# Kernel tuning notes

Measured on AMD Instinct MI355X. Metric: run time of the kernel, lower is better.

## Reference

```python
import jax, jax.numpy as jnp
import numpy as np

N_HEADS = 16

def _rotate_half(t):
    d = t.shape[-1] // 2
    return jnp.concatenate([-t[..., d:], t[..., :d]], axis=-1)

def _apply_rope(t, cos, sin):
    # t: [B,S,H,dh], cos/sin: [S,1,dh] broadcast over B and H
    return t * cos + _rotate_half(t) * sin

def setup_inputs() -> dict:
    key = jax.random.key(0)
    ks = jax.random.split(key, 7)
    B, S, D = 2, 2048, 2048
    dh = D // N_HEADS
    scale = 1.0 / np.sqrt(D)
    return {
        "x": jax.random.normal(ks[0], (B, S, D), dtype=jnp.float32),
        "rope_cos": jax.random.uniform(ks[1], (S, dh), dtype=jnp.float32),
        "rope_sin": jax.random.uniform(ks[2], (S, dh), dtype=jnp.float32),
        "Wq": jax.random.normal(ks[3], (D, D), dtype=jnp.float32) * scale,
        "Wk": jax.random.normal(ks[4], (D, D), dtype=jnp.float32) * scale,
        "Wv": jax.random.normal(ks[5], (D, D), dtype=jnp.float32) * scale,
        "Wo": jax.random.normal(ks[6], (D, D), dtype=jnp.float32) * scale,
    }

def reference(x, rope_cos, rope_sin, Wq, Wk, Wv, Wo):
    B, S, D = x.shape
    H = N_HEADS
    dh = D // H
    # QKV projections (nn.Linear: x @ W.T), reshape to heads
    q = (x @ Wq.T).reshape(B, S, H, dh)
    k = (x @ Wk.T).reshape(B, S, H, dh)
    v = (x @ Wv.T).reshape(B, S, H, dh)
    cos = rope_cos[:, None, :]  # [S,1,dh]
    sin = rope_sin[:, None, :]
    q = _apply_rope(q, cos, sin)
    k = _apply_rope(k, cos, sin)
    # Attention: [B,H,S,S] scores, scaled softmax
    scores = jnp.einsum("bqhd,bkhd->bhqk", q, k) / jnp.sqrt(jnp.asarray(dh, dtype=x.dtype))
    probs = jax.nn.softmax(scores, axis=-1)
    out = jnp.einsum("bhqk,bkhd->bqhd", probs, v).reshape(B, S, D)
    return out @ Wo.T
```

## Files before the change

kernel.cpp:

```cpp
#include <hip/hip_runtime.h>
#include <hip/hip_bf16.h>

typedef unsigned short u16;
typedef __bf16 bf16x8 __attribute__((ext_vector_type(8)));
typedef float f32x4 __attribute__((ext_vector_type(4)));

__device__ __forceinline__ float bf2f(u16 u) {
  union { unsigned int i; float f; } v; v.i = ((unsigned int)u) << 16; return v.f;
}
__device__ __forceinline__ u16 f2bf(float f) {
  union { float f; unsigned int i; } v; v.f = f;
  unsigned int r = v.i + 0x7fffu + ((v.i >> 16) & 1u);
  return (u16)(r >> 16);
}
__device__ __forceinline__ unsigned cvtpk(float lo, float hi) {
  unsigned r;
  asm("v_cvt_pk_bf16_f32 %0, %1, %2" : "=v"(r) : "v"(lo), "v"(hi));
  return r;
}

__device__ __forceinline__ void async_load16(void* lds, const void* g) {
  __builtin_amdgcn_global_load_lds((const __attribute__((address_space(1))) void*)g,
                                   (__attribute__((address_space(3))) void*)lds, 16, 0, 0);
}

__global__ void convert_all(const float* __restrict__ x, const float* __restrict__ Wq,
                            const float* __restrict__ Wk, const float* __restrict__ Wv,
                            const float* __restrict__ Wo, u16* __restrict__ xb,
                            u16* __restrict__ Wqkb, u16* __restrict__ Wvb,
                            u16* __restrict__ Wob) {
  int bid = blockIdx.x;
  const float* src;
  u16* dst;
  int off;
  if (bid < 8192)       { src = x;  dst = xb;              off = bid; }
  else if (bid < 12288) { src = Wq; dst = Wqkb;            off = bid - 8192; }
  else if (bid < 16384) { src = Wk; dst = Wqkb + 4194304;  off = bid - 12288; }
  else if (bid < 20480) { src = Wv; dst = Wvb;             off = bid - 16384; }
  else                  { src = Wo; dst = Wob;             off = bid - 20480; }
  int i = off * 1024 + threadIdx.x * 4;
  float4 v = *(const float4*)(src + i);
  ushort4 o;
  o.x = f2bf(v.x); o.y = f2bf(v.y); o.z = f2bf(v.z); o.w = f2bf(v.w);
  *(ushort4*)(dst + i) = o;
}

template <int BMHALF, int ROPE, int OUT_F32>
__device__ __forceinline__ void gemm_pipe_body(const u16* __restrict__ A,
                                               const u16* __restrict__ Bm,
                                               void* __restrict__ C, int M, int N, int K,
                                               int tm, int tn, u16* lds,
                                               const float* __restrict__ cosb,
                                               const float* __restrict__ sinb,
                                               float qscale) {
  constexpr int MIc = BMHALF / 16;
  constexpr int SUBU16 = (BMHALF == 128) ? 16384 : 12288;
  constexpr int BOFF = (BMHALF == 128) ? 8192 : 4096;
  const int t = threadIdx.x;
  const int w = t >> 6, l = t & 63;
  const int wm = w >> 2, wn = w & 3;
  const int lr = l & 15, lh = l >> 4;
  const size_t row0 = (size_t)tm * (2 * BMHALF), col0 = (size_t)tn * 256;
  const u16* Ag = A + row0 * K;
  const u16* Bg = Bm + col0 * K;

  const int ra = t >> 2;
  const int kcs = ((t & 3) << 3) ^ ((ra & 6) << 2);
  auto stage = [&](int s) {
    u16* dst = lds + (s & 3) * SUBU16;
    const size_t koff = (size_t)s * 32 + kcs;
    if constexpr (BMHALF == 128) {
      async_load16(dst + t * 8,         Ag + (size_t)ra * K + koff);
      async_load16(dst + 4096 + t * 8,  Ag + (size_t)(ra + 128) * K + koff);
      async_load16(dst + 8192 + t * 8,  Bg + (size_t)ra * K + koff);
      async_load16(dst + 12288 + t * 8, Bg + (size_t)(ra + 128) * K + koff);
    } else {
      async_load16(dst + t * 8,         Ag + (size_t)ra * K + koff);
      async_load16(dst + 4096 + t * 8,  Bg + (size_t)ra * K + koff);
      async_load16(dst + 8192 + t * 8,  Bg + (size_t)(ra + 128) * K + koff);
    }
  };
  const int swl = (lh * 8) ^ ((lr & 6) << 2);
  auto read_af = [&](bf16x8* dst, int s) {
    const u16* sub = lds + (s & 3) * SUBU16;
#pragma unroll
    for (int mi = 0; mi < MIc; ++mi)
      dst[mi] = *reinterpret_cast<const bf16x8*>(sub + (wm * BMHALF + mi * 16 + lr) * 32 + swl);
  };
  auto read_bfv = [&](bf16x8* dst, int s) {
    const u16* sub = lds + (s & 3) * SUBU16 + BOFF;
#pragma unroll
    for (int ni = 0; ni < 4; ++ni) {
      int colf = ROPE ? ((wn >> 1) * 128 + (wn & 1) * 32 + (ni >> 1) * 64 + (ni & 1) * 16)
                      : (wn * 64 + ni * 16);
      dst[ni] = *reinterpret_cast<const bf16x8*>(sub + (colf + lr) * 32 + swl);
    }
  };

  f32x4 acc[MIc][4];
#pragma unroll
  for (int i = 0; i < MIc; ++i)
#pragma unroll
    for (int j = 0; j < 4; ++j) acc[i][j] = (f32x4){0.f, 0.f, 0.f, 0.f};

  const int NK = K >> 5;
  bf16x8 afA[MIc], afB[MIc], bfvA[4], bfvB[4];

  stage(0); stage(1); stage(2);
  if constexpr (BMHALF == 128) asm volatile("s_waitcnt vmcnt(8)" ::: "memory");
  else                         asm volatile("s_waitcnt vmcnt(6)" ::: "memory");
  __builtin_amdgcn_s_barrier();
  asm volatile("" ::: "memory");
  read_af(afA, 0);
  read_bfv(bfvA, 0);

  auto pipestep = [&](int s, bf16x8* curA, bf16x8* curB, bf16x8* nxtA, bf16x8* nxtB) {
    if (s + 2 < NK) {
      if constexpr (BMHALF == 128) asm volatile("s_waitcnt vmcnt(4)" ::: "memory");
      else                         asm volatile("s_waitcnt vmcnt(3)" ::: "memory");
    } else {
      asm volatile("s_waitcnt vmcnt(0)" ::: "memory");
    }
    __builtin_amdgcn_s_barrier();
    asm volatile("" ::: "memory");
    if (s + 3 < NK) stage(s + 3);
    if (s + 1 < NK) {
      read_af(nxtA, s + 1);
      read_bfv(nxtB, s + 1);
    }
    __builtin_amdgcn_s_setprio(1);
#pragma unroll
    for (int mi = 0; mi < MIc; ++mi)
#pragma unroll
      for (int ni = 0; ni < 4; ++ni)
        acc[mi][ni] = __builtin_amdgcn_mfma_f32_16x16x32_bf16(curA[mi], curB[ni], acc[mi][ni], 0, 0, 0);
    __builtin_amdgcn_s_setprio(0);
  };

  for (int s = 0; s < NK; s += 2) {
    pipestep(s,     afA, bfvA, afB, bfvB);
    pipestep(s + 1, afB, bfvB, afA, bfvA);
  }

  if constexpr (ROPE) {
    float scale = (2 * tn + (wn >> 1)) < 16 ? qscale : 1.0f;
    size_t colbase = col0 + (wn >> 1) * 128;
#pragma unroll
    for (int mi = 0; mi < MIc; ++mi)
#pragma unroll
      for (int r = 0; r < 4; ++r) {
        size_t row = row0 + wm * BMHALF + mi * 16 + lh * 4 + r;
        int si = (int)(row & 2047);
        const float* cr = cosb + si * 128;
        const float* sr = sinb + si * 128;
#pragma unroll
        for (int ni = 0; ni < 2; ++ni) {
          int dlo = (wn & 1) * 32 + ni * 16 + lr;
          float v0 = acc[mi][ni][r];
          float v1 = acc[mi][ni + 2][r];
          float o0 = (v0 * cr[dlo] - v1 * sr[dlo]) * scale;
          float o1 = (v1 * cr[64 + dlo] + v0 * sr[64 + dlo]) * scale;
          ((u16*)C)[row * N + colbase + dlo]      = f2bf(o0);
          ((u16*)C)[row * N + colbase + 64 + dlo] = f2bf(o1);
        }
      }
  } else {
#pragma unroll
    for (int mi = 0; mi < MIc; ++mi)
#pragma unroll
      for (int ni = 0; ni < 4; ++ni)
#pragma unroll
        for (int r = 0; r < 4; ++r) {
          size_t row = row0 + wm * BMHALF + mi * 16 + lh * 4 + r;
          size_t col = col0 + wn * 64 + ni * 16 + lr;
          float v = acc[mi][ni][r];
          if (OUT_F32)
            ((float*)C)[row * N + col] = v;
          else
            ((u16*)C)[row * N + col] = f2bf(v);
        }
  }
}

__global__ __launch_bounds__(512, 2)
void gemm_qkv256(const u16* __restrict__ xb, const u16* __restrict__ Wqkb,
                 const u16* __restrict__ Wvb, u16* __restrict__ QKb, u16* __restrict__ VTb,
                 const float* __restrict__ cosb, const float* __restrict__ sinb,
                 float qscale) {
  __shared__ __align__(16) u16 lds[4 * 16384];
  int bid = blockIdx.x;
  if (bid < 256) {
    int swz = (bid & 7) * 32 + (bid >> 3);
    gemm_pipe_body<128, 1, 0>(xb, Wqkb, QKb, 4096, 4096, 2048, swz >> 4, swz & 15, lds,
                              cosb, sinb, qscale);
  } else {
    int b2 = bid - 256;
    int swz = (b2 & 7) * 32 + (b2 >> 3);
    gemm_pipe_body<64, 0, 0>(Wvb, xb, VTb, 2048, 4096, 2048, swz >> 4, swz & 15, lds,
                             nullptr, nullptr, 0.f);
  }
}

__global__ __launch_bounds__(512, 2)
void gemm_o(const u16* __restrict__ Ob, const u16* __restrict__ Wob, float* __restrict__ out) {
  __shared__ __align__(16) u16 lds[4 * 16384];
  int bid = blockIdx.x;
  int swz = (bid & 7) * 32 + (bid >> 3);
  gemm_pipe_body<64, 0, 1>(Ob, Wob, (void*)out, 4096, 2048, 2048, swz >> 3, swz & 7, lds,
                           nullptr, nullptr, 0.f);
}

__global__ __launch_bounds__(256, 2)
void attn_kernel(const u16* __restrict__ QKb, const u16* __restrict__ VT,
                 u16* __restrict__ Ob) {
  __shared__ __align__(16) u16 sK[2][64 * 128];
  __shared__ __align__(16) u16 sV[2][128 * 64];
  __shared__ __align__(16) u16 sP[4][32 * 64];

  int id = blockIdx.x;
  int swz = (id & 7) * 64 + (id >> 3);
  int bh = swz >> 4;
  int qb = swz & 15;
  int b = bh >> 4, h = bh & 15;
  int t = threadIdx.x, w = t >> 6, l = t & 63;
  int lr = l & 15, lh = l >> 4;
  int lr7 = lr & 7;
  int q0 = qb * 128;

  const u16* Kbase = QKb + (size_t)(b * 2048) * 4096 + 2048 + h * 128;
  const u16* Vbase = VT + (size_t)(h * 128) * 4096 + b * 2048;
  u16* sPw = sP[w];

  bf16x8 aq[2][4];
#pragma unroll
  for (int qf = 0; qf < 2; ++qf) {
    size_t qrow = (size_t)(b * 2048 + q0 + w * 32 + qf * 16 + lr) * 4096 + h * 128;
#pragma unroll
    for (int c = 0; c < 4; ++c)
      aq[qf][c] = *reinterpret_cast<const bf16x8*>(QKb + qrow + c * 32 + lh * 8);
  }

  f32x4 zero = {0.f, 0.f, 0.f, 0.f};
  f32x4 acc_o[2][8];
#pragma unroll
  for (int qf = 0; qf < 2; ++qf)
#pragma unroll
    for (int d = 0; d < 8; ++d) acc_o[qf][d] = zero;
  float m_row[2] = {-1e30f, -1e30f};
  float l_row[2] = {0.f, 0.f};

  auto stage = [&](int buf, int kt2) {
    const u16* Kt = Kbase + (size_t)(kt2 * 64) * 4096;
    const u16* Vt = Vbase + kt2 * 64;
#pragma unroll
    for (int it = 0; it < 4; ++it) {
      int o = it * 4096 + t * 16;
      int rowK = o >> 8;
      int cbK = (o & 255) ^ ((rowK & 7) << 4);
      async_load16((u16*)sK[buf] + (o >> 1), Kt + (size_t)rowK * 4096 + (cbK >> 1));
      int rowV = o >> 7;
      int cbV = (o & 127) ^ ((rowV & 7) << 4);
      async_load16((u16*)sV[buf] + (o >> 1), Vt + (size_t)rowV * 4096 + (cbV >> 1));
    }
  };

  stage(0, 0);
  __syncthreads();
  int cur = 0;

  for (int kt = 0; kt < 32; ++kt) {
    if (kt < 31) stage(cur ^ 1, kt + 1);

    const u16* sKc = sK[cur];
    const u16* sVc = sV[cur];

    f32x4 sacc[2][4];
#pragma unroll
    for (int qf = 0; qf < 2; ++qf)
#pragma unroll
      for (int g = 0; g < 4; ++g) sacc[qf][g] = zero;
#pragma unroll
    for (int g = 0; g < 4; ++g) {
      int row = g * 16 + lr;
      int xr = lr7 << 4;
#pragma unroll
      for (int c = 0; c < 4; ++c) {
        int cb = (c * 64 + lh * 16) ^ xr;
        bf16x8 bk = *reinterpret_cast<const bf16x8*>(sKc + row * 128 + (cb >> 1));
        sacc[0][g] = __builtin_amdgcn_mfma_f32_16x16x32_bf16(bk, aq[0][c], sacc[0][g], 0, 0, 0);
        sacc[1][g] = __builtin_amdgcn_mfma_f32_16x16x32_bf16(bk, aq[1][c], sacc[1][g], 0, 0, 0);
      }
    }

#pragma unroll
    for (int qf = 0; qf < 2; ++qf) {
      f32x4 m4;
#pragma unroll
      for (int e = 0; e < 4; ++e)
        m4[e] = fmaxf(fmaxf(sacc[qf][0][e], sacc[qf][1][e]),
                      fmaxf(sacc[qf][2][e], sacc[qf][3][e]));
      float mx = fmaxf(fmaxf(m4[0], m4[1]), fmaxf(m4[2], m4[3]));
      mx = fmaxf(mx, __shfl_xor(mx, 16));
      mx = fmaxf(mx, __shfl_xor(mx, 32));
      float mo = m_row[qf];
      if (!__all(mx <= mo + 8.f)) {
        float mn = fmaxf(mo, mx);
        float al = __builtin_amdgcn_exp2f(mo - mn);
        m_row[qf] = mn;
        l_row[qf] *= al;
#pragma unroll
        for (int d = 0; d < 8; ++d) acc_o[qf][d] *= al;
      }
      float mn = m_row[qf];
#pragma unroll
      for (int g = 0; g < 4; ++g)
#pragma unroll
        for (int e = 0; e < 4; ++e)
          sacc[qf][g][e] = __builtin_amdgcn_exp2f(sacc[qf][g][e] - mn);
      f32x4 s4;
#pragma unroll
      for (int e = 0; e < 4; ++e)
        s4[e] = (sacc[qf][0][e] + sacc[qf][1][e]) + (sacc[qf][2][e] + sacc[qf][3][e]);
      float rs = (s4[0] + s4[1]) + (s4[2] + s4[3]);
      rs += __shfl_xor(rs, 16);
      rs += __shfl_xor(rs, 32);
      l_row[qf] += rs;

      int rowb = (qf * 16 + lr) * 128;
      int xw = lr7 << 4;
#pragma unroll
      for (int g = 0; g < 4; ++g) {
        uint2 pw;
        pw.x = cvtpk(sacc[qf][g][0], sacc[qf][g][1]);
        pw.y = cvtpk(sacc[qf][g][2], sacc[qf][g][3]);
        int cb = (g * 32 + lh * 8) ^ xw;
        *reinterpret_cast<uint2*>(reinterpret_cast<char*>(sPw) + rowb + cb) = pw;
      }
    }

    bf16x8 bp[2][2];
#pragma unroll
    for (int qf = 0; qf < 2; ++qf) {
      int rowb = (qf * 16 + lr) * 128;
      int xr = lr7 << 4;
#pragma unroll
      for (int c2 = 0; c2 < 2; ++c2) {
        int cb = (c2 * 64 + lh * 16) ^ xr;
        bp[qf][c2] = *reinterpret_cast<const bf16x8*>(
            reinterpret_cast<const char*>(sPw) + rowb + cb);
      }
    }
#pragma unroll
    for (int c2 = 0; c2 < 2; ++c2) {
#pragma unroll
      for (int d = 0; d < 8; ++d) {
        int row = d * 16 + lr;
        int cb = (c2 * 64 + lh * 16) ^ (lr7 << 4);
        bf16x8 bv = *reinterpret_cast<const bf16x8*>(sVc + row * 64 + (cb >> 1));
        acc_o[0][d] = __builtin_amdgcn_mfma_f32_16x16x32_bf16(bv, bp[0][c2], acc_o[0][d], 0, 0, 0);
        acc_o[1][d] = __builtin_amdgcn_mfma_f32_16x16x32_bf16(bv, bp[1][c2], acc_o[1][d], 0, 0, 0);
      }
    }

    __syncthreads();
    cur ^= 1;
  }

#pragma unroll
  for (int qf = 0; qf < 2; ++qf) {
    float inv = 1.f / l_row[qf];
    size_t qrow = (size_t)(b * 2048 + q0 + w * 32 + qf * 16 + lr) * 2048 + h * 128;
#pragma unroll
    for (int d = 0; d < 8; ++d) {
      ushort4 o;
      o.x = f2bf(acc_o[qf][d][0] * inv);
      o.y = f2bf(acc_o[qf][d][1] * inv);
      o.z = f2bf(acc_o[qf][d][2] * inv);
      o.w = f2bf(acc_o[qf][d][3] * inv);
      *reinterpret_cast<ushort4*>(Ob + qrow + d * 16 + lh * 4) = o;
    }
  }
}

extern "C" void kernel_launch(void* const* d_in, const int* in_sizes, int n_in,
                              void* d_out, int out_size, void* d_ws, size_t ws_size,
                              hipStream_t stream) {
  const float* x  = (const float*)d_in[0];
  const float* rc = (const float*)d_in[1];
  const float* rs = (const float*)d_in[2];
  const float* Wq = (const float*)d_in[3];
  const float* Wk = (const float*)d_in[4];
  const float* Wv = (const float*)d_in[5];
  const float* Wo = (const float*)d_in[6];
  float* out = (float*)d_out;
  char* ws = (char*)d_ws;
  const size_t MB = 1024 * 1024;
  u16* xb   = (u16*)(ws);
  u16* Wqkb = (u16*)(ws + 16 * MB);
  u16* Wvb  = (u16*)(ws + 32 * MB);
  u16* Wob  = (u16*)(ws + 40 * MB);
  u16* QKb  = (u16*)(ws + 48 * MB);
  u16* VTb  = (u16*)(ws + 80 * MB);
  u16* Ob   = (u16*)(ws + 16 * MB);

  convert_all<<<24576, 256, 0, stream>>>(x, Wq, Wk, Wv, Wo, xb, Wqkb, Wvb, Wob);

  const float qscale = 0.08838834764831845f * 1.4426950408889634f;
  gemm_qkv256<<<512, 512, 0, stream>>>(xb, Wqkb, Wvb, QKb, VTb, rc, rs, qscale);

  attn_kernel<<<512, 256, 0, stream>>>(QKb, VTb, Ob);

  gemm_o<<<256, 512, 0, stream>>>(Ob, Wob, out);
}
```

Baseline: 249.3 us.

## Replace QK projection GEMM with 8-phase K=64 double-buffered pipeline

The QK-projection path (256x256 tiles with fused RoPE) moves from the generic 4-stage K=32 pipeline to a dedicated routine. The new routine uses K=64 steps, double-buffered LDS halves loaded by quarter-tiles, and splits each step into four MFMA sub-blocks separated by barriers. The aim is to interleave global-to-LDS loads and fragment reads with MFMA work at finer granularity and to cut the number of K iterations. In exchange it adds many more barriers per iteration, and the lower LDS footprint of gemm_o could change occupancy.

Measured after the change: 244.6 us. No clear change (-1.9%).

```diff
diff --git a/kernel.cpp b/kernel.cpp
--- a/kernel.cpp
+++ b/kernel.cpp
@@ -23,6 +23,9 @@
   __builtin_amdgcn_global_load_lds((const __attribute__((address_space(1))) void*)g,
                                    (__attribute__((address_space(3))) void*)lds, 16, 0, 0);
 }
+
+#define BARRIER() do { asm volatile("" ::: "memory"); __builtin_amdgcn_s_barrier(); \
+                       asm volatile("" ::: "memory"); } while (0)
 
 __global__ void convert_all(const float* __restrict__ x, const float* __restrict__ Wq,
                             const float* __restrict__ Wk, const float* __restrict__ Wv,
@@ -45,14 +48,139 @@
   *(ushort4*)(dst + i) = o;
 }
 
-template <int BMHALF, int ROPE, int OUT_F32>
-__device__ __forceinline__ void gemm_pipe_body(const u16* __restrict__ A,
+__device__ __forceinline__ void gemm_qk_8phase(const u16* __restrict__ A,
                                                const u16* __restrict__ Bm,
-                                               void* __restrict__ C, int M, int N, int K,
+                                               u16* __restrict__ C, int K,
                                                int tm, int tn, u16* lds,
                                                const float* __restrict__ cosb,
                                                const float* __restrict__ sinb,
                                                float qscale) {
+  const int NK = K >> 6;
+  const int t = threadIdx.x;
+  const int w = t >> 6, l = t & 63;
+  const int wm = w >> 2, wn = w & 3;
+  const int lr = l & 15, lh = l >> 4;
+  const size_t row0 = (size_t)tm * 256, col0 = (size_t)tn * 256;
+  const u16* Ag = A + row0 * K;
+  const u16* Bg = Bm + col0 * K;
+
+  auto stage_half = [&](int T, int h) {
+    u16* dst = lds + (T & 1) * 32768 + h * 8192;
+    const u16* src = (h < 2) ? (Ag + (size_t)(h * 128) * K)
+                             : (Bg + (size_t)((h - 2) * 128) * K);
+    const int kb = T * 64;
+#pragma unroll
+    for (int it = 0; it < 2; ++it) {
+      int o = it * 8192 + t * 16;
+      int r = o >> 7;
+      int cbs = (o & 127) ^ ((r & 7) << 4);
+      async_load16(dst + (o >> 1), src + (size_t)r * K + kb + (cbs >> 1));
+    }
+  };
+
+  bf16x8 afq[4][2], bLo[2][2], bHi[2][2];
+  f32x4 acc[8][4];
+#pragma unroll
+  for (int i = 0; i < 8; ++i)
+#pragma unroll
+    for (int j = 0; j < 4; ++j) acc[i][j] = (f32x4){0.f, 0.f, 0.f, 0.f};
+
+  auto read_a = [&](int T, int mh) {
+    const u16* sub = lds + (T & 1) * 32768 + wm * 8192;
+#pragma unroll
+    for (int mi = 0; mi < 4; ++mi) {
+      int r = (mh * 4 + mi) * 16 + lr;
+      int bb = r * 128, xr = (r & 7) << 4;
+#pragma unroll
+      for (int ks = 0; ks < 2; ++ks)
+        afq[mi][ks] = *reinterpret_cast<const bf16x8*>(
+            sub + ((bb + ((ks * 64 + lh * 16) ^ xr)) >> 1));
+    }
+  };
+  auto read_b = [&](bf16x8 (*dst)[2], int T, int nh) {
+    const u16* sub = lds + (T & 1) * 32768 + (2 + (wn >> 1)) * 8192;
+#pragma unroll
+    for (int nj2 = 0; nj2 < 2; ++nj2) {
+      int nj = nh * 2 + nj2;
+      int c = (wn & 1) * 32 + (nj & 1) * 16 + (nj >> 1) * 64 + lr;
+      int bb = c * 128, xr = (c & 7) << 4;
+#pragma unroll
+      for (int ks = 0; ks < 2; ++ks)
+        dst[nj2][ks] = *reinterpret_cast<const bf16x8*>(
+            sub + ((bb + ((ks * 64 + lh * 16) ^ xr)) >> 1));
+    }
+  };
+  auto mfma_q = [&](bf16x8 (*bq)[2], int mh, int nh) {
+    __builtin_amdgcn_s_setprio(1);
+#pragma unroll
+    for (int ks = 0; ks < 2; ++ks)
+#pragma unroll
+      for (int mi = 0; mi < 4; ++mi)
+#pragma unroll
+        for (int nj2 = 0; nj2 < 2; ++nj2)
+          acc[mh * 4 + mi][nh * 2 + nj2] = __builtin_amdgcn_mfma_f32_16x16x32_bf16(
+              afq[mi][ks], bq[nj2][ks], acc[mh * 4 + mi][nh * 2 + nj2], 0, 0, 0);
+    __builtin_amdgcn_s_setprio(0);
+  };
+
+  stage_half(0, 2); stage_half(0, 0); stage_half(0, 1); stage_half(0, 3);
+  stage_half(1, 2); stage_half(1, 0);
+  asm volatile("s_waitcnt vmcnt(4)" ::: "memory");
+  BARRIER();
+
+  for (int T = 0; T < NK; ++T) {
+    read_a(T, 0);
+    read_b(bLo, T, 0);
+    if (T + 1 < NK) stage_half(T + 1, 1);
+    BARRIER();
+    mfma_q(bLo, 0, 0);
+    BARRIER();
+    read_b(bHi, T, 1);
+    if (T + 1 < NK) stage_half(T + 1, 3);
+    BARRIER();
+    mfma_q(bHi, 0, 1);
+    BARRIER();
+    read_a(T, 1);
+    if (T + 2 < NK) stage_half(T + 2, 2);
+    BARRIER();
+    mfma_q(bLo, 1, 0);
+    BARRIER();
+    if (T + 2 < NK) stage_half(T + 2, 0);
+    if (T + 1 <= NK - 2)      asm volatile("s_waitcnt vmcnt(4)" ::: "memory");
+    else if (T + 1 == NK - 1) asm volatile("s_waitcnt vmcnt(0)" ::: "memory");
+    BARRIER();
+    mfma_q(bHi, 1, 1);
+    BARRIER();
+  }
+
+  float scale = (2 * tn + (wn >> 1)) < 16 ? qscale : 1.0f;
+  size_t colbase = col0 + (wn >> 1) * 128;
+#pragma unroll
+  for (int mi = 0; mi < 8; ++mi)
+#pragma unroll
+    for (int r = 0; r < 4; ++r) {
+      size_t row = row0 + wm * 128 + mi * 16 + lh * 4 + r;
+      int si = (int)(row & 2047);
+      const float* cr = cosb + si * 128;
+      const float* sr = sinb + si * 128;
+#pragma unroll
+      for (int ni = 0; ni < 2; ++ni) {
+        int dlo = (wn & 1) * 32 + ni * 16 + lr;
+        float v0 = acc[mi][ni][r];
+        float v1 = acc[mi][ni + 2][r];
+        float o0 = (v0 * cr[dlo] - v1 * sr[dlo]) * scale;
+        float o1 = (v1 * cr[64 + dlo] + v0 * sr[64 + dlo]) * scale;
+        C[row * 4096 + colbase + dlo]      = f2bf(o0);
+        C[row * 4096 + colbase + 64 + dlo] = f2bf(o1);
+      }
+    }
+}
+
+template <int BMHALF, int OUT_F32>
+__device__ __forceinline__ void gemm_pipe_body(const u16* __restrict__ A,
+                                               const u16* __restrict__ Bm,
+                                               void* __restrict__ C, int M, int N, int K,
+                                               int tm, int tn, u16* lds) {
   constexpr int MIc = BMHALF / 16;
   constexpr int SUBU16 = (BMHALF == 128) ? 16384 : 12288;
   constexpr int BOFF = (BMHALF == 128) ? 8192 : 4096;
@@ -90,11 +218,8 @@
   auto read_bfv = [&](bf16x8* dst, int s) {
     const u16* sub = lds + (s & 3) * SUBU16 + BOFF;
 #pragma unroll
-    for (int ni = 0; ni < 4; ++ni) {
-      int colf = ROPE ? ((wn >> 1) * 128 + (wn & 1) * 32 + (ni >> 1) * 64 + (ni & 1) * 16)
-                      : (wn * 64 + ni * 16);
-      dst[ni] = *reinterpret_cast<const bf16x8*>(sub + (colf + lr) * 32 + swl);
-    }
+    for (int ni = 0; ni < 4; ++ni)
+      dst[ni] = *reinterpret_cast<const bf16x8*>(sub + (wn * 64 + ni * 16 + lr) * 32 + swl);
   };
 
   f32x4 acc[MIc][4];
@@ -109,8 +234,7 @@
   stage(0); stage(1); stage(2);
   if constexpr (BMHALF == 128) asm volatile("s_waitcnt vmcnt(8)" ::: "memory");
   else                         asm volatile("s_waitcnt vmcnt(6)" ::: "memory");
-  __builtin_amdgcn_s_barrier();
-  asm volatile("" ::: "memory");
+  BARRIER();
   read_af(afA, 0);
   read_bfv(bfvA, 0);
 
@@ -121,8 +245,7 @@
     } else {
       asm volatile("s_waitcnt vmcnt(0)" ::: "memory");
     }
-    __builtin_amdgcn_s_barrier();
-    asm volatile("" ::: "memory");
+    BARRIER();
     if (s + 3 < NK) stage(s + 3);
     if (s + 1 < NK) {
       read_af(nxtA, s + 1);
@@ -142,44 +265,20 @@
     pipestep(s + 1, afB, bfvB, afA, bfvA);
   }
 
-  if constexpr (ROPE) {
-    float scale = (2 * tn + (wn >> 1)) < 16 ? qscale : 1.0f;
-    size_t colbase = col0 + (wn >> 1) * 128;
-#pragma unroll
-    for (int mi = 0; mi < MIc; ++mi)
+#pragma unroll
+  for (int mi = 0; mi < MIc; ++mi)
+#pragma unroll
+    for (int ni = 0; ni < 4; ++ni)
 #pragma unroll
       for (int r = 0; r < 4; ++r) {
         size_t row = row0 + wm * BMHALF + mi * 16 + lh * 4 + r;
-        int si = (int)(row & 2047);
-        const float* cr = cosb + si * 128;
-        const float* sr = sinb + si * 128;
-#pragma unroll
-        for (int ni = 0; ni < 2; ++ni) {
-          int dlo = (wn & 1) * 32 + ni * 16 + lr;
-          float v0 = acc[mi][ni][r];
-          float v1 = acc[mi][ni + 2][r];
-          float o0 = (v0 * cr[dlo] - v1 * sr[dlo]) * scale;
-          float o1 = (v1 * cr[64 + dlo] + v0 * sr[64 + dlo]) * scale;
-          ((u16*)C)[row * N + colbase + dlo]      = f2bf(o0);
-          ((u16*)C)[row * N + colbase + 64 + dlo] = f2bf(o1);
-        }
-      }
-  } else {
-#pragma unroll
-    for (int mi = 0; mi < MIc; ++mi)
-#pragma unroll
-      for (int ni = 0; ni < 4; ++ni)
-#pragma unroll
-        for (int r = 0; r < 4; ++r) {
-          size_t row = row0 + wm * BMHALF + mi * 16 + lh * 4 + r;
-          size_t col = col0 + wn * 64 + ni * 16 + lr;
-          float v = acc[mi][ni][r];
-          if (OUT_F32)
-            ((float*)C)[row * N + col] = v;
-          else
-            ((u16*)C)[row * N + col] = f2bf(v);
-        }
-  }
+        size_t col = col0 + wn * 64 + ni * 16 + lr;
+        float v = acc[mi][ni][r];
+        if (OUT_F32)
+          ((float*)C)[row * N + col] = v;
+        else
+          ((u16*)C)[row * N + col] = f2bf(v);
+      }
 }
 
 __global__ __launch_bounds__(512, 2)
@@ -187,27 +286,24 @@
                  const u16* __restrict__ Wvb, u16* __restrict__ QKb, u16* __restrict__ VTb,
                  const float* __restrict__ cosb, const float* __restrict__ sinb,
                  float qscale) {
-  __shared__ __align__(16) u16 lds[4 * 16384];
+  __shared__ __align__(16) u16 lds[65536];
   int bid = blockIdx.x;
   if (bid < 256) {
     int swz = (bid & 7) * 32 + (bid >> 3);
-    gemm_pipe_body<128, 1, 0>(xb, Wqkb, QKb, 4096, 4096, 2048, swz >> 4, swz & 15, lds,
-                              cosb, sinb, qscale);
+    gemm_qk_8phase(xb, Wqkb, QKb, 2048, swz >> 4, swz & 15, lds, cosb, sinb, qscale);
   } else {
     int b2 = bid - 256;
     int swz = (b2 & 7) * 32 + (b2 >> 3);
-    gemm_pipe_body<64, 0, 0>(Wvb, xb, VTb, 2048, 4096, 2048, swz >> 4, swz & 15, lds,
-                             nullptr, nullptr, 0.f);
+    gemm_pipe_body<64, 0>(Wvb, xb, VTb, 2048, 4096, 2048, swz >> 4, swz & 15, lds);
   }
 }
 
 __global__ __launch_bounds__(512, 2)
 void gemm_o(const u16* __restrict__ Ob, const u16* __restrict__ Wob, float* __restrict__ out) {
-  __shared__ __align__(16) u16 lds[4 * 16384];
+  __shared__ __align__(16) u16 lds[4 * 12288];
   int bid = blockIdx.x;
   int swz = (bid & 7) * 32 + (bid >> 3);
-  gemm_pipe_body<64, 0, 1>(Ob, Wob, (void*)out, 4096, 2048, 2048, swz >> 3, swz & 7, lds,
-                           nullptr, nullptr, 0.f);
+  gemm_pipe_body<64, 1>(Ob, Wob, (void*)out, 4096, 2048, 2048, swz >> 3, swz & 7, lds);
 }
 
 __global__ __launch_bounds__(256, 2)
```
